# Optimization experiments

Hardware: AMD Instinct MI355X
Metric: run time of the kernel (lower is better)

The kernel has to match this reference:

```python
import jax, jax.numpy as jnp
import numpy as np

NUM_TAGS = 48
B, S = 512, 2048


def setup_inputs() -> dict:
    key = jax.random.key(0)
    k1, k2, k3, k4, k5 = jax.random.split(key, 5)
    emissions = jax.random.normal(k1, (B, S, NUM_TAGS), dtype=jnp.float32)
    tags = jax.random.randint(k2, (B, S), 0, NUM_TAGS, dtype=jnp.int32)
    mask = jnp.ones((B, S), dtype=jnp.float32)
    transitions = jax.random.uniform(k3, (NUM_TAGS, NUM_TAGS), minval=-0.1, maxval=0.1, dtype=jnp.float32)
    start_transitions = jax.random.uniform(k4, (NUM_TAGS,), minval=-0.1, maxval=0.1, dtype=jnp.float32)
    end_transitions = jax.random.uniform(k5, (NUM_TAGS,), minval=-0.1, maxval=0.1, dtype=jnp.float32)
    return {"emissions": emissions, "transitions": transitions,
            "start_transitions": start_transitions, "end_transitions": end_transitions,
            "tags": tags, "mask": mask}


def reference(emissions, transitions, start_transitions, end_transitions, tags, mask):
    # emissions: [B,S,T], tags: [B,S] int, mask: [B,S] float (1 = valid)
    b, s, t = emissions.shape
    barange = jnp.arange(b)

    # ---- gold path score (fully vectorized over time) ----
    emit = jnp.take_along_axis(emissions, tags[:, :, None], axis=2)[..., 0]  # [B,S]
    score = start_transitions[tags[:, 0]] + emit[:, 0]
    trans = transitions[tags[:, :-1], tags[:, 1:]]                            # [B,S-1]
    score = score + jnp.sum((trans + emit[:, 1:]) * mask[:, 1:], axis=1)
    last_idx = mask.sum(axis=1).astype(jnp.int32) - 1
    last_tags = tags[barange, last_idx]
    score = score + end_transitions[last_tags]

    # ---- log-partition via forward algorithm (scan over time) ----
    alpha0 = start_transitions[None, :] + emissions[:, 0]                     # [B,T]

    def step(alpha, xs):
        emit_t, mask_t = xs                                                   # [B,T], [B]
        # scores[b,i,j] = alpha[b,i] + transitions[i,j] + emit_t[b,j]
        scores = alpha[:, :, None] + transitions[None, :, :] + emit_t[:, None, :]
        next_alpha = jax.nn.logsumexp(scores, axis=1)                         # [B,T]
        m = mask_t[:, None]
        alpha = next_alpha * m + alpha * (1.0 - m)
        return alpha, None

    xs = (jnp.swapaxes(emissions[:, 1:], 0, 1), jnp.swapaxes(mask[:, 1:], 0, 1))
    alpha, _ = jax.lax.scan(step, alpha0, xs)
    partition = jax.nn.logsumexp(alpha + end_transitions[None, :], axis=1)    # [B]

    return -jnp.mean(score - partition)
```

## Files before the change

### kernel.cpp

```cpp
#include <hip/hip_runtime.h>

#define NTAGS 48
#define NB    512
#define SLEN  2048


__device__ __forceinline__ float rl_f(float v, int l) {
  return __builtin_bit_cast(float, __builtin_amdgcn_readlane(__builtin_bit_cast(int, v), l));
}

template <int CTRL, bool BC>
__device__ __forceinline__ float dpp_mv(float oldv, float v) {
  return __builtin_bit_cast(float, __builtin_amdgcn_update_dpp(
      __builtin_bit_cast(int, oldv), __builtin_bit_cast(int, v), CTRL, 0xF, 0xF, BC));
}

__device__ __forceinline__ float wred_max(float v) {
  v = fmaxf(v, dpp_mv<0x128, false>(v, v));
  v = fmaxf(v, dpp_mv<0x124, false>(v, v));
  v = fmaxf(v, dpp_mv<0x122, false>(v, v));
  v = fmaxf(v, dpp_mv<0x121, false>(v, v));
  v = fmaxf(v, dpp_mv<0x142, false>(v, v));
  v = fmaxf(v, dpp_mv<0x143, false>(v, v));
  return rl_f(v, 63);
}

__device__ __forceinline__ float wred_sum(float v) {
  v += dpp_mv<0x128, true>(0.0f, v);
  v += dpp_mv<0x124, true>(0.0f, v);
  v += dpp_mv<0x122, true>(0.0f, v);
  v += dpp_mv<0x121, true>(0.0f, v);
  v += dpp_mv<0x142, true>(0.0f, v);
  v += dpp_mv<0x143, true>(0.0f, v);
  return rl_f(v, 63);
}

__device__ __forceinline__ float rdot48(float v, const float* Ev) {
  float a0 = 0.f, a1 = 0.f, a2 = 0.f, a3 = 0.f;
#pragma unroll
  for (int i = 0; i < NTAGS; i += 4) {
    a0 = fmaf(rl_f(v, i + 0), Ev[i + 0], a0);
    a1 = fmaf(rl_f(v, i + 1), Ev[i + 1], a1);
    a2 = fmaf(rl_f(v, i + 2), Ev[i + 2], a2);
    a3 = fmaf(rl_f(v, i + 3), Ev[i + 3], a3);
  }
  return (a0 + a1) + (a2 + a3);
}

__device__ __forceinline__ void renorm(float& p, float& cl) {
  float mx = wred_max(p);
  int e = ((__builtin_bit_cast(int, mx) >> 23) & 255) - 127;
  float r = __builtin_bit_cast(float, (127 - e) << 23);
  p *= r;
  cl += (float)e * 0.6931471805599453f;
}


extern "C" __global__ __launch_bounds__(64, 1)
void crf_main(const float* __restrict__ emis,
              const float* __restrict__ trans,
              const float* __restrict__ startt,
              const float* __restrict__ endt,
              const int*   __restrict__ tags,
              const float* __restrict__ mask,
              float* __restrict__ wa, float* __restrict__ wb,
              float* __restrict__ wsc, int* __restrict__ wcnt) {
  __shared__ float st[NTAGS * NTAGS];
  const int lane = threadIdx.x;
  const int bid  = blockIdx.x;

  if (bid >= 2 * NB) {
    const int b = bid - 2 * NB;
    for (int k = lane; k < NTAGS * NTAGS; k += 64) st[k] = trans[k];
    __syncthreads();
    const int* tb = tags + (size_t)b * SLEN;
    float ssum = 0.0f, csum = 0.0f;
    for (int it = 0; it < SLEN / 64; ++it) {
      const int t   = it * 64 + lane;
      int   cur = tb[t];
      float mv  = mask[(size_t)b * SLEN + t];
      float ev  = emis[((size_t)b * SLEN + t) * NTAGS + cur];
      float s;
      if (t == 0) {
        s = startt[cur] + ev;
      } else {
        int prev = tb[t - 1];
        s = (mv != 0.0f) ? (st[prev * NTAGS + cur] + ev) : 0.0f;
      }
      ssum += s;
      csum += (mv != 0.0f) ? 1.0f : 0.0f;
    }
    ssum = wred_sum(ssum);
    csum = wred_sum(csum);
    if (lane == 0) { wsc[b] = ssum; wcnt[b] = (int)(csum + 0.5f); }
    return;
  }

  const int  b   = bid >> 1;
  const bool fwd = (bid & 1) == 0;
  const int  jc  = lane < NTAGS ? lane : (NTAGS - 1);

  const float* eb = emis + (size_t)b * SLEN * NTAGS;
  const float* mb = mask + (size_t)b * SLEN;

  float Ev[NTAGS];
  if (fwd) {
#pragma unroll
    for (int i = 0; i < NTAGS; ++i) Ev[i] = __expf(trans[i * NTAGS + jc]);
  } else {
#pragma unroll
    for (int j = 0; j < NTAGS; ++j) Ev[j] = __expf(trans[jc * NTAGS + j]);
  }

  float ebuf[8];
  float p, cl, een;

  if (fwd) {
    float a0 = startt[jc] + eb[jc];
    if (lane >= NTAGS) a0 = -1e30f;
    float m0 = wred_max(a0);
    p  = __expf(a0 - m0);
    cl = m0;
#pragma unroll
    for (int k = 1; k <= 8; ++k) ebuf[k & 7] = eb[(size_t)k * NTAGS + jc];
    een = __expf(ebuf[1]);

    for (int g = 0; g < 128; ++g) {
#pragma unroll
      for (int u = 0; u < 8; ++u) {
        const int t = 1 + 8 * g + u;
        float ee = een;
        een = __expf(ebuf[(t + 1) & 7]);
        float acc = rdot48(p, Ev);
        float mv  = mb[t];
        float pn  = acc * ee;
        p = (mv != 0.0f) ? pn : p;
        ebuf[t & 7] = eb[(size_t)(t + 8) * NTAGS + jc];
        if (u == 7) renorm(p, cl);
      }
    }
    if (lane < NTAGS) wa[b * NTAGS + lane] = __logf(p) + cl;
  } else {
    float b0 = endt[jc];
    if (lane >= NTAGS) b0 = -1e30f;
    float m0 = wred_max(b0);
    p  = __expf(b0 - m0);
    cl = m0;
#pragma unroll
    for (int k = 0; k < 8; ++k) ebuf[(2047 - k) & 7] = eb[(size_t)(2047 - k) * NTAGS + jc];
    float q = p * __expf(ebuf[7]);
    een = __expf(ebuf[6]);

#pragma unroll
    for (int pt = 0; pt < 7; ++pt) {
      const int t = 2047 - pt;
      float ee = een;
      een = __expf(ebuf[(t + 6) & 7]);
      float acc = rdot48(q, Ev);
      float mv  = mb[t];
      p = (mv != 0.0f) ? acc : p;
      ebuf[t & 7] = eb[(size_t)(t - 8) * NTAGS + jc];
      if (pt == 6) renorm(p, cl);
      q = p * ee;
    }
    for (int g = 0; g < 127; ++g) {
#pragma unroll
      for (int u = 0; u < 8; ++u) {
        const int t = 2040 - 8 * g - u;
        float ee = een;
        een = __expf(ebuf[(t + 6) & 7]);
        float acc = rdot48(q, Ev);
        float mv  = mb[t];
        p = (mv != 0.0f) ? acc : p;
        ebuf[t & 7] = eb[(size_t)(t - 8) * NTAGS + jc];
        if (u == 7) renorm(p, cl);
        q = p * ee;
      }
    }
    if (lane < NTAGS) wb[b * NTAGS + lane] = __logf(p) + cl;
  }
}


extern "C" __global__ __launch_bounds__(64)
void crf_combine(const float* __restrict__ wa, const float* __restrict__ wb,
                 const float* __restrict__ wsc, const int* __restrict__ wcnt,
                 const int* __restrict__ tags, const float* __restrict__ endt,
                 float* __restrict__ out) {
  const int b    = blockIdx.x;
  const int lane = threadIdx.x;
  float v = -1e30f;
  if (lane < NTAGS) v = wa[b * NTAGS + lane] + wb[b * NTAGS + lane];
  float m = wred_max(v);
  float s = wred_sum(__expf(v - m));
  float part = m + __logf(s);
  int   last = wcnt[b] - 1;
  float score = wsc[b] + endt[tags[(size_t)b * SLEN + last]];
  if (lane == 0) atomicAdd(out, (part - score) * (1.0f / (float)NB));
}


extern "C" void kernel_launch(void* const* d_in, const int* in_sizes, int n_in,
                              void* d_out, int out_size, void* d_ws, size_t ws_size,
                              hipStream_t stream) {
  const float* emis  = (const float*)d_in[0];
  const float* trans = (const float*)d_in[1];
  const float* stt   = (const float*)d_in[2];
  const float* ent   = (const float*)d_in[3];
  const int*   tags  = (const int*)d_in[4];
  const float* mask  = (const float*)d_in[5];

  float* wa   = (float*)d_ws;
  float* wb   = wa + NB * NTAGS;
  float* wsc  = wb + NB * NTAGS;
  int*   wcnt = (int*)(wsc + NB);

  hipMemsetAsync(d_out, 0, sizeof(float), stream);
  crf_main<<<2 * NB + NB, 64, 0, stream>>>(emis, trans, stt, ent, tags, mask,
                                           wa, wb, wsc, wcnt);
  crf_combine<<<NB, 64, 0, stream>>>(wa, wb, wsc, wcnt, tags, ent, (float*)d_out);
}
```

Measured before the change: 425.4 us.

## Batch 16 sequences per wave and run CRF recurrence on bf16 MFMA

```diff
diff --git a/kernel.cpp b/kernel.cpp
--- a/kernel.cpp
+++ b/kernel.cpp
@@ -3,6 +3,11 @@
 #define NTAGS 48
 #define NB    512
 #define SLEN  2048
+
+typedef short  short8 __attribute__((ext_vector_type(8)));
+typedef float  f32x4  __attribute__((ext_vector_type(4)));
+typedef unsigned u32x4 __attribute__((ext_vector_type(4)));
+typedef unsigned u32x2 __attribute__((ext_vector_type(2)));
 
 
 __device__ __forceinline__ float rl_f(float v, int l) {
@@ -35,24 +40,76 @@
   return rl_f(v, 63);
 }
 
-__device__ __forceinline__ float rdot48(float v, const float* Ev) {
-  float a0 = 0.f, a1 = 0.f, a2 = 0.f, a3 = 0.f;
-#pragma unroll
-  for (int i = 0; i < NTAGS; i += 4) {
-    a0 = fmaf(rl_f(v, i + 0), Ev[i + 0], a0);
-    a1 = fmaf(rl_f(v, i + 1), Ev[i + 1], a1);
-    a2 = fmaf(rl_f(v, i + 2), Ev[i + 2], a2);
-    a3 = fmaf(rl_f(v, i + 3), Ev[i + 3], a3);
-  }
-  return (a0 + a1) + (a2 + a3);
-}
-
-__device__ __forceinline__ void renorm(float& p, float& cl) {
-  float mx = wred_max(p);
-  int e = ((__builtin_bit_cast(int, mx) >> 23) & 255) - 127;
+__device__ __forceinline__ void quad_mix(unsigned a, unsigned b, unsigned& Z, unsigned& W) {
+#if __has_builtin(__builtin_amdgcn_permlane32_swap) && __has_builtin(__builtin_amdgcn_permlane16_swap)
+  u32x2 uv = __builtin_amdgcn_permlane32_swap(a, b, false, false);
+  u32x2 zw = __builtin_amdgcn_permlane16_swap(uv[0], uv[1], false, false);
+  Z = zw[0]; W = zw[1];
+#else
+  const int lane = threadIdx.x & 63;
+  const int c = lane & 15;
+  const int hi = (lane >> 4) & 1;
+  const int s1 = (c + hi * 32) << 2;
+  const int s2 = (c + 16 + hi * 32) << 2;
+  unsigned za = __builtin_amdgcn_ds_bpermute(s1, a);
+  unsigned zb = __builtin_amdgcn_ds_bpermute(s1, b);
+  unsigned wa_ = __builtin_amdgcn_ds_bpermute(s2, a);
+  unsigned wb_ = __builtin_amdgcn_ds_bpermute(s2, b);
+  Z = (lane < 32) ? za : zb;
+  W = (lane < 32) ? wa_ : wb_;
+#endif
+}
+
+__device__ __forceinline__ unsigned bpack_tr(float x, float y) {
+  return __builtin_amdgcn_perm(__builtin_bit_cast(unsigned, y),
+                               __builtin_bit_cast(unsigned, x), 0x07060302u);
+}
+__device__ __forceinline__ unsigned bpack_rne(float x, float y) {
+  unsigned ux = __builtin_bit_cast(unsigned, x);
+  unsigned uy = __builtin_bit_cast(unsigned, y);
+  ux += 0x7FFFu + ((ux >> 16) & 1u);
+  uy += 0x7FFFu + ((uy >> 16) & 1u);
+  return (ux >> 16) | (uy & 0xFFFF0000u);
+}
+
+__device__ __forceinline__ void p_to_b(const float* P, u32x4& B0, u32x4& B1) {
+  unsigned d00 = bpack_tr(P[0], P[1]);
+  unsigned d01 = bpack_tr(P[2], P[3]);
+  unsigned d10 = bpack_tr(P[4], P[5]);
+  unsigned d11 = bpack_tr(P[6], P[7]);
+  unsigned d20 = bpack_tr(P[8], P[9]);
+  unsigned d21 = bpack_tr(P[10], P[11]);
+  unsigned b0, b1, b2, b3, b4, b5, b6, b7;
+  quad_mix(d00, d10, b0, b2);
+  quad_mix(d01, d11, b1, b3);
+  quad_mix(d20, d20, b4, b6);
+  quad_mix(d21, d21, b5, b7);
+  B0[0] = b0; B0[1] = b1; B0[2] = b2; B0[3] = b3;
+  B1[0] = b4; B1[1] = b5; B1[2] = b6; B1[3] = b7;
+}
+
+__device__ __forceinline__ float quad_max(float m) {
+  unsigned z, w;
+  quad_mix(__builtin_bit_cast(unsigned, m), __builtin_bit_cast(unsigned, m), z, w);
+  m = fmaxf(__builtin_bit_cast(float, z), __builtin_bit_cast(float, w));
+  quad_mix(__builtin_bit_cast(unsigned, m), __builtin_bit_cast(unsigned, m), z, w);
+  return fmaxf(__builtin_bit_cast(float, z), __builtin_bit_cast(float, w));
+}
+
+__device__ __forceinline__ void renorm12(float* P, float& cl) {
+  float m = P[0];
+#pragma unroll
+  for (int i = 1; i < 12; ++i) m = fmaxf(m, P[i]);
+  m = quad_max(m);
+  int e = ((__builtin_bit_cast(int, m) >> 23) & 255) - 127;
   float r = __builtin_bit_cast(float, (127 - e) << 23);
-  p *= r;
+#pragma unroll
+  for (int i = 0; i < 12; ++i) P[i] *= r;
   cl += (float)e * 0.6931471805599453f;
+}
+
+__device__ __forceinline__ f32x4 mfma16(short8 a, short8 b, f32x4 c) {
+  return __builtin_amdgcn_mfma_f32_16x16x32_bf16(a, b, c, 0, 0, 0);
 }
 
 
@@ -69,14 +126,14 @@
   const int lane = threadIdx.x;
   const int bid  = blockIdx.x;
 
-  if (bid >= 2 * NB) {
-    const int b = bid - 2 * NB;
+  if (bid >= 64) {
+    const int b = bid - 64;
     for (int k = lane; k < NTAGS * NTAGS; k += 64) st[k] = trans[k];
     __syncthreads();
     const int* tb = tags + (size_t)b * SLEN;
     float ssum = 0.0f, csum = 0.0f;
     for (int it = 0; it < SLEN / 64; ++it) {
-      const int t   = it * 64 + lane;
+      const int t = it * 64 + lane;
       int   cur = tb[t];
       float mv  = mask[(size_t)b * SLEN + t];
       float ev  = emis[((size_t)b * SLEN + t) * NTAGS + cur];
@@ -96,88 +153,212 @@
     return;
   }
 
-  const int  b   = bid >> 1;
-  const bool fwd = (bid & 1) == 0;
-  const int  jc  = lane < NTAGS ? lane : (NTAGS - 1);
+  const bool fwd = bid < 32;
+  const int  b0  = (fwd ? bid : bid - 32) * 16;
+  const int  l   = lane & 15;
+  const int  q   = lane >> 4;
+  const int  b   = b0 + l;
 
   const float* eb = emis + (size_t)b * SLEN * NTAGS;
   const float* mb = mask + (size_t)b * SLEN;
 
-  float Ev[NTAGS];
+  short8 Af[3][2];
+#pragma unroll
+  for (int tt = 0; tt < 3; ++tt) {
+#pragma unroll
+    for (int h = 0; h < 2; ++h) {
+      u32x4 dw;
+#pragma unroll
+      for (int d = 0; d < 4; ++d) {
+        int k0 = 8 * q + 2 * d;
+        int i0 = 32 * h + k0;
+        float x, y;
+        if (fwd) {
+          x = (i0 < 48)     ? __expf(trans[i0 * NTAGS + 16 * tt + l])       : 0.0f;
+          y = (i0 + 1 < 48) ? __expf(trans[(i0 + 1) * NTAGS + 16 * tt + l]) : 0.0f;
+        } else {
+          x = (i0 < 48)     ? __expf(trans[(16 * tt + l) * NTAGS + i0])     : 0.0f;
+          y = (i0 + 1 < 48) ? __expf(trans[(16 * tt + l) * NTAGS + i0 + 1]) : 0.0f;
+        }
+        dw[d] = bpack_rne(x, y);
+      }
+      Af[tt][h] = __builtin_bit_cast(short8, dw);
+    }
+  }
+
+  f32x4 ring[8][3];
+  float mbuf[8];
+  float P[12];
+  float ee[12];
+  float cl;
+  u32x4 B0, B1;
+  const f32x4 zf = {0.f, 0.f, 0.f, 0.f};
+
   if (fwd) {
-#pragma unroll
-    for (int i = 0; i < NTAGS; ++i) Ev[i] = __expf(trans[i * NTAGS + jc]);
+    float a0[12], ml;
+#pragma unroll
+    for (int tt = 0; tt < 3; ++tt) {
+      f32x4 ev = *(const f32x4*)(eb + 16 * tt + 4 * q);
+      f32x4 sv = *(const f32x4*)(startt + 16 * tt + 4 * q);
+#pragma unroll
+      for (int r = 0; r < 4; ++r) a0[4 * tt + r] = sv[r] + ev[r];
+    }
+    ml = a0[0];
+#pragma unroll
+    for (int i = 1; i < 12; ++i) ml = fmaxf(ml, a0[i]);
+    ml = quad_max(ml);
+#pragma unroll
+    for (int i = 0; i < 12; ++i) P[i] = __expf(a0[i] - ml);
+    cl = ml;
+    p_to_b(P, B0, B1);
+
+#pragma unroll
+    for (int k = 1; k <= 8; ++k) {
+#pragma unroll
+      for (int tt = 0; tt < 3; ++tt)
+        ring[k & 7][tt] = *(const f32x4*)(eb + (size_t)k * NTAGS + 16 * tt + 4 * q);
+      mbuf[k & 7] = mb[k];
+    }
+#pragma unroll
+    for (int tt = 0; tt < 3; ++tt)
+#pragma unroll
+      for (int r = 0; r < 4; ++r) ee[4 * tt + r] = __expf(ring[1][tt][r]);
+
+    for (int g = 0; g < 128; ++g) {
+#pragma unroll
+      for (int u = 0; u < 8; ++u) {
+        const int t  = 1 + 8 * g + u;
+        const int sl = t & 7, sl1 = (t + 1) & 7;
+        float een[12];
+#pragma unroll
+        for (int tt = 0; tt < 3; ++tt)
+#pragma unroll
+          for (int r = 0; r < 4; ++r) een[4 * tt + r] = __expf(ring[sl1][tt][r]);
+        f32x4 a0v = mfma16(Af[0][0], __builtin_bit_cast(short8, B0), zf);
+        f32x4 a1v = mfma16(Af[1][0], __builtin_bit_cast(short8, B0), zf);
+        f32x4 a2v = mfma16(Af[2][0], __builtin_bit_cast(short8, B0), zf);
+        a0v = mfma16(Af[0][1], __builtin_bit_cast(short8, B1), a0v);
+        a1v = mfma16(Af[1][1], __builtin_bit_cast(short8, B1), a1v);
+        a2v = mfma16(Af[2][1], __builtin_bit_cast(short8, B1), a2v);
+        float mv = mbuf[sl];
+        bool live = (mv != 0.0f);
+        float nP[12];
+#pragma unroll
+        for (int r = 0; r < 4; ++r) {
+          nP[r]     = a0v[r] * ee[r];
+          nP[4 + r] = a1v[r] * ee[4 + r];
+          nP[8 + r] = a2v[r] * ee[8 + r];
+        }
+        if (__all(live)) {
+#pragma unroll
+          for (int i = 0; i < 12; ++i) P[i] = nP[i];
+        } else {
+#pragma unroll
+          for (int i = 0; i < 12; ++i) P[i] = live ? nP[i] : P[i];
+        }
+#pragma unroll
+        for (int tt = 0; tt < 3; ++tt)
+          ring[sl][tt] = *(const f32x4*)(eb + (size_t)(t + 8) * NTAGS + 16 * tt + 4 * q);
+        mbuf[sl] = mb[t + 8];
+        if (u == 7) renorm12(P, cl);
+        p_to_b(P, B0, B1);
+#pragma unroll
+        for (int i = 0; i < 12; ++i) ee[i] = een[i];
+      }
+    }
+#pragma unroll
+    for (int tt = 0; tt < 3; ++tt) {
+      f32x4 o;
+#pragma unroll
+      for (int r = 0; r < 4; ++r) o[r] = __logf(P[4 * tt + r]) + cl;
+      *(f32x4*)(wa + (size_t)b * NTAGS + 16 * tt + 4 * q) = o;
+    }
   } else {
-#pragma unroll
-    for (int j = 0; j < NTAGS; ++j) Ev[j] = __expf(trans[jc * NTAGS + j]);
-  }
-
-  float ebuf[8];
-  float p, cl, een;
-
-  if (fwd) {
-    float a0 = startt[jc] + eb[jc];
-    if (lane >= NTAGS) a0 = -1e30f;
-    float m0 = wred_max(a0);
-    p  = __expf(a0 - m0);
-    cl = m0;
-#pragma unroll
-    for (int k = 1; k <= 8; ++k) ebuf[k & 7] = eb[(size_t)k * NTAGS + jc];
-    een = __expf(ebuf[1]);
-
-    for (int g = 0; g < 128; ++g) {
-#pragma unroll
-      for (int u = 0; u < 8; ++u) {
-        const int t = 1 + 8 * g + u;
-        float ee = een;
-        een = __expf(ebuf[(t + 1) & 7]);
-        float acc = rdot48(p, Ev);
-        float mv  = mb[t];
-        float pn  = acc * ee;
-        p = (mv != 0.0f) ? pn : p;
-        ebuf[t & 7] = eb[(size_t)(t + 8) * NTAGS + jc];
-        if (u == 7) renorm(p, cl);
-      }
-    }
-    if (lane < NTAGS) wa[b * NTAGS + lane] = __logf(p) + cl;
-  } else {
-    float b0 = endt[jc];
-    if (lane >= NTAGS) b0 = -1e30f;
-    float m0 = wred_max(b0);
-    p  = __expf(b0 - m0);
-    cl = m0;
-#pragma unroll
-    for (int k = 0; k < 8; ++k) ebuf[(2047 - k) & 7] = eb[(size_t)(2047 - k) * NTAGS + jc];
-    float q = p * __expf(ebuf[7]);
-    een = __expf(ebuf[6]);
-
-#pragma unroll
-    for (int pt = 0; pt < 7; ++pt) {
-      const int t = 2047 - pt;
-      float ee = een;
-      een = __expf(ebuf[(t + 6) & 7]);
-      float acc = rdot48(q, Ev);
-      float mv  = mb[t];
-      p = (mv != 0.0f) ? acc : p;
-      ebuf[t & 7] = eb[(size_t)(t - 8) * NTAGS + jc];
-      if (pt == 6) renorm(p, cl);
-      q = p * ee;
-    }
+    float a0[12], ml;
+#pragma unroll
+    for (int tt = 0; tt < 3; ++tt) {
+      f32x4 sv = *(const f32x4*)(endt + 16 * tt + 4 * q);
+#pragma unroll
+      for (int r = 0; r < 4; ++r) a0[4 * tt + r] = sv[r];
+    }
+    ml = a0[0];
+#pragma unroll
+    for (int i = 1; i < 12; ++i) ml = fmaxf(ml, a0[i]);
+    ml = quad_max(ml);
+#pragma unroll
+    for (int i = 0; i < 12; ++i) P[i] = __expf(a0[i] - ml);
+    cl = ml;
+
+#pragma unroll
+    for (int k = 0; k < 8; ++k) {
+      const int t = 2047 - k;
+#pragma unroll
+      for (int tt = 0; tt < 3; ++tt)
+        ring[t & 7][tt] = *(const f32x4*)(eb + (size_t)t * NTAGS + 16 * tt + 4 * q);
+      mbuf[t & 7] = mb[t];
+    }
+#pragma unroll
+    for (int tt = 0; tt < 3; ++tt)
+#pragma unroll
+      for (int r = 0; r < 4; ++r) ee[4 * tt + r] = __expf(ring[7][tt][r]);
+
+#define BWD_STEP(T, DO_RENORM)                                                        \
+    {                                                                                 \
+      const int t = (T);                                                              \
+      const int sl = t & 7, slm = (t - 1) & 7;                                        \
+      float een[12];                                                                  \
+      _Pragma("unroll")                                                               \
+      for (int tt = 0; tt < 3; ++tt)                                                  \
+        _Pragma("unroll")                                                             \
+        for (int r = 0; r < 4; ++r) een[4 * tt + r] = __expf(ring[slm][tt][r]);       \
+      float Q[12];                                                                    \
+      _Pragma("unroll")                                                               \
+      for (int i = 0; i < 12; ++i) Q[i] = P[i] * ee[i];                               \
+      p_to_b(Q, B0, B1);                                                              \
+      f32x4 a0v = mfma16(Af[0][0], __builtin_bit_cast(short8, B0), zf);               \
+      f32x4 a1v = mfma16(Af[1][0], __builtin_bit_cast(short8, B0), zf);               \
+      f32x4 a2v = mfma16(Af[2][0], __builtin_bit_cast(short8, B0), zf);               \
+      a0v = mfma16(Af[0][1], __builtin_bit_cast(short8, B1), a0v);                    \
+      a1v = mfma16(Af[1][1], __builtin_bit_cast(short8, B1), a1v);                    \
+      a2v = mfma16(Af[2][1], __builtin_bit_cast(short8, B1), a2v);                    \
+      float mv = mbuf[sl];                                                            \
+      bool live = (mv != 0.0f);                                                       \
+      float nP[12];                                                                   \
+      _Pragma("unroll")                                                               \
+      for (int r = 0; r < 4; ++r) {                                                   \
+        nP[r] = a0v[r]; nP[4 + r] = a1v[r]; nP[8 + r] = a2v[r];                       \
+      }                                                                               \
+      if (__all(live)) {                                                              \
+        _Pragma("unroll")                                                             \
+        for (int i = 0; i < 12; ++i) P[i] = nP[i];                                    \
+      } else {                                                                        \
+        _Pragma("unroll")                                                             \
+        for (int i = 0; i < 12; ++i) P[i] = live ? nP[i] : P[i];                      \
+      }                                                                               \
+      _Pragma("unroll")                                                               \
+      for (int tt = 0; tt < 3; ++tt)                                                  \
+        ring[sl][tt] = *(const f32x4*)(eb + (size_t)(t - 8) * NTAGS + 16 * tt + 4 * q); \
+      mbuf[sl] = mb[t - 8];                                                           \
+      if (DO_RENORM) renorm12(P, cl);                                                 \
+      _Pragma("unroll")                                                               \
+      for (int i = 0; i < 12; ++i) ee[i] = een[i];                                    \
+    }
+
+#pragma unroll
+    for (int pt = 0; pt < 7; ++pt) BWD_STEP(2047 - pt, pt == 6)
     for (int g = 0; g < 127; ++g) {
 #pragma unroll
-      for (int u = 0; u < 8; ++u) {
-        const int t = 2040 - 8 * g - u;
-        float ee = een;
-        een = __expf(ebuf[(t + 6) & 7]);
-        float acc = rdot48(q, Ev);
-        float mv  = mb[t];
-        p = (mv != 0.0f) ? acc : p;
-        ebuf[t & 7] = eb[(size_t)(t - 8) * NTAGS + jc];
-        if (u == 7) renorm(p, cl);
-        q = p * ee;
-      }
-    }
-    if (lane < NTAGS) wb[b * NTAGS + lane] = __logf(p) + cl;
+      for (int u = 0; u < 8; ++u) BWD_STEP(2040 - 8 * g - u, u == 7)
+    }
+#undef BWD_STEP
+
+#pragma unroll
+    for (int tt = 0; tt < 3; ++tt) {
+      f32x4 o;
+#pragma unroll
+      for (int r = 0; r < 4; ++r) o[r] = __logf(P[4 * tt + r]) + cl;
+      *(f32x4*)(wb + (size_t)b * NTAGS + 16 * tt + 4 * q) = o;
+    }
   }
 }
 
@@ -216,7 +397,7 @@
   int*   wcnt = (int*)(wsc + NB);
 
   hipMemsetAsync(d_out, 0, sizeof(float), stream);
-  crf_main<<<2 * NB + NB, 64, 0, stream>>>(emis, trans, stt, ent, tags, mask,
-                                           wa, wb, wsc, wcnt);
+  crf_main<<<64 + NB, 64, 0, stream>>>(emis, trans, stt, ent, tags, mask,
+                                       wa, wb, wsc, wcnt);
   crf_combine<<<NB, 64, 0, stream>>>(wa, wb, wsc, wcnt, tags, ent, (float*)d_out);
 }
```

After: 474.0 us. +11.4%, slower.
